# Kernel tuning notes

Hardware: AMD Instinct MI355X
Metric: run time of the kernel (lower is better)

The kernel has to match this reference:

```python
import jax, jax.numpy as jnp
import numpy as np

B, H, W = 4, 128, 128
THRESHOLD = 0.1      # hard-coded in chamfer_distance_batch
CHUNK = 2048         # row-chunk size for the online-min over the distance matrix
BIG = 1e9            # masks out inactive columns in the min-reduction
EMPTY_CHD = 1e6      # sentinel when either point set is empty (matches torch code)
EPS = 1e-12          # sqrt clamp for numerical safety


def setup_inputs() -> dict:
    key = jax.random.key(0)
    k1, k2 = jax.random.split(key)
    batch1 = jax.random.normal(k1, (B, H, W), dtype=jnp.float32)
    batch2 = jax.random.normal(k2, (B, H, W), dtype=jnp.float32)
    return {"batch1": batch1, "batch2": batch2}


def _chamfer(batch1, batch2):
    Bn, Hn, Wn = batch1.shape
    HW = Hn * Wn
    w1 = jax.nn.relu(batch1 - THRESHOLD).reshape(Bn, HW)   # [B, HW]
    w2 = jax.nn.relu(batch2 - THRESHOLD).reshape(Bn, HW)
    gy, gx = jnp.meshgrid(jnp.arange(Hn), jnp.arange(Wn), indexing='ij')
    coords = jnp.stack([gy, gx], axis=-1).reshape(HW, 2).astype(jnp.float32)  # [HW, 2]
    # torch code multiplies coords by the relu'd weights BEFORE cdist (quirk kept)
    c1 = coords[None, :, :] * w1[:, :, None]               # [B, HW, 2]
    c2 = coords[None, :, :] * w2[:, :, None]
    m1 = w1 > 0                                            # active-point masks
    m2 = w2 > 0

    def directed(cf, mf, ct, mt):
        # mean over active rows of min distance to active columns, chunked
        ct_sq = jnp.sum(ct * ct, axis=-1)                  # [HW]

        def chunk_min(cc):                                 # cc: [CHUNK, 2]
            # |a-b|^2 = |a|^2 + |b|^2 - 2 a.b  (GEMM form)
            d2 = (jnp.sum(cc * cc, axis=-1)[:, None]
                  + ct_sq[None, :]
                  - 2.0 * cc @ ct.T)                       # [CHUNK, HW]
            d = jnp.sqrt(jnp.maximum(d2, EPS))
            return jnp.min(jnp.where(mt[None, :], d, BIG), axis=1)  # [CHUNK]

        mins = jax.lax.map(chunk_min, cf.reshape(-1, CHUNK, 2)).reshape(-1)  # [HW]
        n = jnp.sum(mf)
        return jnp.sum(mins * mf) / jnp.maximum(n, 1)

    def per_image(c1b, m1b, c2b, m2b):
        chd = directed(c1b, m1b, c2b, m2b) + directed(c2b, m2b, c1b, m1b)
        nonempty = (jnp.sum(m1b) > 0) & (jnp.sum(m2b) > 0)
        return jnp.where(nonempty, chd, jnp.asarray(EMPTY_CHD, chd.dtype))

    return jax.vmap(per_image)(c1, m1, c2, m2)   # [B]


def reference(batch1, batch2):
    return _chamfer(batch1, batch2)
```

## Files before the change

kernel.cpp:

```cpp
#include <hip/hip_runtime.h>
#include <math.h>


#define B_ 4
#define HW_ 16384
#define THRESH 0.1f
#define BIGF 1e30f
#define EPS_ 1e-12f

#define SEGCAP 4096
#define NSEG 4
#define NBIN 256
#define BINSCALE 0.25f
#define BINW 4.0f
#define RG 128
#define NW 8
#define AWIN 1024
#define PD_NGRP 128

__global__ __launch_bounds__(1024)
void compact_kernel(const float* __restrict__ in1, const float* __restrict__ in2,
                    int* __restrict__ segcounts, float4* __restrict__ pts,
                    uint4* __restrict__ minarr4, int* __restrict__ histG) {
    int seg = blockIdx.x, combo = blockIdx.y;
    int b = combo >> 1, s = combo & 1;
    int tid = threadIdx.x, lane = tid & 63, wid = tid >> 6;
    const float* in = s ? in2 : in1;
    int ibase = seg * SEGCAP + tid * 4;
    float4 v = ((const float4*)(in + b * HW_))[(unsigned)ibase >> 2];
    float w0 = v.x - THRESH, w1 = v.y - THRESH, w2 = v.z - THRESH, w3 = v.w - THRESH;
    int a0 = w0 > 0.f, a1 = w1 > 0.f, a2 = w2 > 0.f, a3 = w3 > 0.f;

    unsigned int bb = __float_as_uint(BIGF);
    minarr4[(unsigned)(combo * HW_ + ibase) >> 2] = make_uint4(bb, bb, bb, bb);

    __shared__ int hist[NBIN];
    if (tid < NBIN) hist[tid] = 0;

    int c = a0 + a1 + a2 + a3;
    int incl = c;
#pragma unroll
    for (int o = 1; o < 64; o <<= 1) {
        int x = __shfl_up(incl, o, 64);
        if (lane >= o) incl += x;
    }
    int wexcl = incl - c;
    __shared__ int wtot[16], wpre[17];
    if (lane == 63) wtot[wid] = incl;
    __syncthreads();
    if (tid == 0) {
        int run = 0;
#pragma unroll
        for (int ww = 0; ww < 16; ++ww) { wpre[ww] = run; run += wtot[ww]; }
        wpre[16] = run;
    }
    __syncthreads();
    int off = wpre[wid] + wexcl;
    float4* dst = pts + combo * HW_ + seg * SEGCAP;
    float wv[4] = {w0, w1, w2, w3};
    int   av[4] = {a0, a1, a2, a3};
#pragma unroll
    for (int u = 0; u < 4; ++u) {
        if (av[u]) {
            int i = ibase + u;
            float qx = (float)(i >> 7) * wv[u];
            float qy = (float)(i & 127) * wv[u];
            float zz = qx * qx + qy * qy;
            dst[off] = make_float4(qx, qy, zz, 0.0f);
            int bin = min(NBIN - 1, (int)(sqrtf(zz) * BINSCALE));
            atomicAdd(&hist[bin], 1);
            ++off;
        }
    }
    if (tid == 0) segcounts[combo * 4 + seg] = wpre[16];
    __syncthreads();
    if (tid < NBIN)
        histG[(combo * NSEG + seg) * NBIN + tid] = hist[tid];
}

__global__ __launch_bounds__(512)
void scatter_kernel(const int* __restrict__ segcounts, const float4* __restrict__ pts,
                    const int* __restrict__ histG, float4* __restrict__ sorted,
                    int* __restrict__ binstartG) {
    int seg = blockIdx.x, combo = blockIdx.y;
    int tid = threadIdx.x;
    __shared__ int h[NSEG][NBIN];
    __shared__ int sc[NBIN];
    __shared__ int cur[NBIN];
    for (int i = tid; i < NSEG * NBIN; i += 512)
        h[i >> 8][i & 255] = histG[combo * NSEG * NBIN + i];
    __syncthreads();
    if (tid < NBIN) sc[tid] = h[0][tid] + h[1][tid] + h[2][tid] + h[3][tid];
    __syncthreads();
#pragma unroll
    for (int o = 1; o < NBIN; o <<= 1) {
        int v = (tid < NBIN && tid >= o) ? sc[tid - o] : 0;
        __syncthreads();
        if (tid < NBIN) sc[tid] += v;
        __syncthreads();
    }
    if (tid < NBIN) {
        int tot = h[0][tid] + h[1][tid] + h[2][tid] + h[3][tid];
        int excl = sc[tid] - tot;
        int o2 = excl;
        for (int s2 = 0; s2 < seg; ++s2) o2 += h[s2][tid];
        cur[tid] = o2;
        if (seg == 0) binstartG[combo * (NBIN + 1) + tid] = excl;
    }
    if (seg == 0 && tid == 0)
        binstartG[combo * (NBIN + 1) + NBIN] = sc[NBIN - 1];
    __syncthreads();
    int c = segcounts[combo * 4 + seg];
    const float4* src = pts + combo * HW_ + seg * SEGCAP;
    for (int i = tid; i < c; i += 512) {
        float4 p = src[i];
        int bin = min(NBIN - 1, (int)(sqrtf(p.z) * BINSCALE));
        int idx = atomicAdd(&cur[bin], 1);
        sorted[(size_t)combo * HW_ + idx] =
            make_float4(p.x, p.y, p.z, __uint_as_float((unsigned)(seg * SEGCAP + i)));
    }
}

__global__ __launch_bounds__(512, 4)
void pdist_kernel(const float4* __restrict__ sorted, const int* __restrict__ binstart,
                  unsigned int* __restrict__ minarr) {
    int grp = blockIdx.x, combo = blockIdx.y;
    int tid = threadIdx.x, lane = tid & 63, w = tid >> 6;
    int tc = combo ^ 1;
    int n_from = binstart[combo * (NBIN + 1) + NBIN];
    int n_to   = binstart[tc * (NBIN + 1) + NBIN];
    if (n_from <= 0 || n_to <= 0) return;
    int rbase = grp * RG;
    if (rbase >= n_from) return;

    const float4* __restrict__ rows = sorted + (size_t)combo * HW_;
    const float4* __restrict__ cols = sorted + (size_t)tc * HW_;

    int r0 = rbase + lane, r1 = rbase + 64 + lane;
    bool v0 = r0 < n_from, v1 = r1 < n_from;
    float4 P0 = rows[min(r0, n_from - 1)];
    float4 P1 = rows[min(r1, n_from - 1)];
    float npx0 = -2.0f * P0.x, npy0 = -2.0f * P0.y, p20 = P0.z;
    float npx1 = -2.0f * P1.x, npy1 = -2.0f * P1.y, p21 = P1.z;
    unsigned int slot0 = __float_as_uint(P0.w);
    unsigned int slot1 = __float_as_uint(P1.w);
    float m0 = BIGF, m1 = BIGF;

    int blo_r = min(NBIN - 1, (int)(sqrtf(rows[rbase].z) * BINSCALE));
    int bhi_r = min(NBIN - 1, (int)(sqrtf(rows[min(rbase + RG - 1, n_from - 1)].z) * BINSCALE));
    float rho_lo = (float)blo_r * BINW;
    float rho_hi = (float)(bhi_r + 1) * BINW;

    int jmid = (binstart[tc * (NBIN + 1) + blo_r]
                + binstart[tc * (NBIN + 1) + min(bhi_r + 1, NBIN)]) >> 1;
    int aHi = min(n_to, jmid + AWIN / 2);
    int aLo = max(0, aHi - AWIN);
    aHi = min(n_to, aLo + AWIN);

    __shared__ __align__(16) float bx[NW][64], by[NW][64], bz[NW][64];
    __shared__ float mW[NW][RG];

    auto ld = [&](int jb) -> float4 {
        int j = jb + lane;
        return (j < n_to) ? cols[j] : make_float4(0.0f, 0.0f, BIGF, 0.0f);
    };
    auto proc = [&](float4 qc) {
        bx[w][lane] = qc.x; by[w][lane] = qc.y; bz[w][lane] = qc.z;
        const float4* X = (const float4*)bx[w];
        const float4* Y = (const float4*)by[w];
        const float4* Z = (const float4*)bz[w];
#pragma unroll
        for (int q4 = 0; q4 < 16; ++q4) {
            float4 qx = X[q4], qy = Y[q4], qz = Z[q4];
            float t0 = fmaf(qy.x, npy0, fmaf(qx.x, npx0, qz.x));
            float u1 = fmaf(qy.y, npy0, fmaf(qx.y, npx0, qz.y));
            m0 = fminf(m0, fminf(t0, u1));
            float u2 = fmaf(qy.z, npy0, fmaf(qx.z, npx0, qz.z));
            float u3 = fmaf(qy.w, npy0, fmaf(qx.w, npx0, qz.w));
            m0 = fminf(m0, fminf(u2, u3));
            float s0 = fmaf(qy.x, npy1, fmaf(qx.x, npx1, qz.x));
            float s1 = fmaf(qy.y, npy1, fmaf(qx.y, npx1, qz.y));
            m1 = fminf(m1, fminf(s0, s1));
            float s2 = fmaf(qy.z, npy1, fmaf(qx.z, npx1, qz.z));
            float s3 = fmaf(qy.w, npy1, fmaf(qx.w, npx1, qz.w));
            m1 = fminf(m1, fminf(s2, s3));
        }
    };

    int nbA = (aHi - aLo + 63) >> 6;
    float4 qn = (w < nbA) ? ld(aLo + (w << 6))
                          : make_float4(0.0f, 0.0f, BIGF, 0.0f);
    for (int bi = w; bi < nbA; bi += NW) {
        float4 qc = qn;
        if (bi + NW < nbA) qn = ld(aLo + ((bi + NW) << 6));
        proc(qc);
    }

    mW[w][lane] = m0; mW[w][64 + lane] = m1;
    __syncthreads();
    float c0 = mW[0][lane], c1 = mW[0][64 + lane];
#pragma unroll
    for (int ww = 1; ww < NW; ++ww) {
        c0 = fminf(c0, mW[ww][lane]);
        c1 = fminf(c1, mW[ww][64 + lane]);
    }
    float md0 = v0 ? fmaxf(c0 + p20, 0.0f) : -1.0f;
    float md1 = v1 ? fmaxf(c1 + p21, 0.0f) : -1.0f;
    float g = fmaxf(md0, md1);
#pragma unroll
    for (int o = 1; o < 64; o <<= 1) g = fmaxf(g, __shfl_xor(g, o));

    float S = sqrtf((g + 1.0f) * (1.0f / 0.99f)) * 1.001f;
    int b_lo = max(0, (int)((rho_lo - S) * BINSCALE) - 1);
    int b_hi = min(NBIN, (int)((rho_hi + S) * BINSCALE) + 2);
    int jlo2 = binstart[tc * (NBIN + 1) + b_lo];
    int jhi2 = binstart[tc * (NBIN + 1) + b_hi];

    m0 = c0; m1 = c1;
    int nbL = (max(0, aLo - jlo2) + 63) >> 6;
    int nbR = (max(0, jhi2 - aHi) + 63) >> 6;
    int nbB = nbL + nbR;
    auto jbB = [&](int bi) {
        return (bi < nbL) ? (jlo2 + (bi << 6)) : (aHi + ((bi - nbL) << 6));
    };
    qn = (w < nbB) ? ld(jbB(w)) : make_float4(0.0f, 0.0f, BIGF, 0.0f);
    for (int bi = w; bi < nbB; bi += NW) {
        float4 qc = qn;
        if (bi + NW < nbB) qn = ld(jbB(bi + NW));
        proc(qc);
    }
    __syncthreads();
    mW[w][lane] = m0; mW[w][64 + lane] = m1;
    __syncthreads();
    if (w == 0) {
        float f0 = mW[0][lane], f1 = mW[0][64 + lane];
#pragma unroll
        for (int ww = 1; ww < NW; ++ww) {
            f0 = fminf(f0, mW[ww][lane]);
            f1 = fminf(f1, mW[ww][64 + lane]);
        }
        if (v0) minarr[combo * HW_ + slot0] = __float_as_uint(fmaxf(f0 + p20, 0.0f));
        if (v1) minarr[combo * HW_ + slot1] = __float_as_uint(fmaxf(f1 + p21, 0.0f));
    }
}

__global__ void reduce_out_kernel(const int* __restrict__ segcounts,
                                  const unsigned int* __restrict__ minarr,
                                  float* __restrict__ out) {
    int b = blockIdx.x;
    int tid = threadIdx.x;
    int d = tid >> 9;
    int t = tid & 511;
    int combo = b * 2 + d;

    float acc = 0.0f;
    for (int s = 0; s < NSEG; ++s) {
        int c = segcounts[combo * 4 + s];
        const unsigned int* ma = minarr + combo * HW_ + s * SEGCAP;
        for (int r = t; r < c; r += 512)
            acc += sqrtf(fmaxf(__uint_as_float(ma[r]), EPS_));
    }
#pragma unroll
    for (int o = 32; o >= 1; o >>= 1) acc += __shfl_down(acc, o);

    __shared__ float wsum[16];
    if ((tid & 63) == 0) wsum[tid >> 6] = acc;
    __syncthreads();
    if (tid == 0) {
        float s0 = 0.0f, s1 = 0.0f;
#pragma unroll
        for (int w = 0; w < 8; ++w)  s0 += wsum[w];
#pragma unroll
        for (int w = 8; w < 16; ++w) s1 += wsum[w];
        int n0 = 0, n1 = 0;
#pragma unroll
        for (int s = 0; s < NSEG; ++s) {
            n0 += segcounts[(b * 2) * 4 + s];
            n1 += segcounts[(b * 2 + 1) * 4 + s];
        }
        out[b] = (n0 > 0 && n1 > 0)
                 ? s0 / (float)n0 + s1 / (float)n1
                 : 1.0e6f;
    }
}

extern "C" void kernel_launch(void* const* d_in, const int* in_sizes, int n_in,
                              void* d_out, int out_size, void* d_ws, size_t ws_size,
                              hipStream_t stream) {
    const float* in1 = (const float*)d_in[0];
    const float* in2 = (const float*)d_in[1];
    float* out = (float*)d_out;
    char* ws = (char*)d_ws;
    int* segcounts = (int*)ws;
    float4* pts = (float4*)(ws + 256);
    size_t minoff = 256 + (size_t)8 * HW_ * sizeof(float4);
    unsigned int* minarr = (unsigned int*)(ws + minoff);
    size_t sortoff = minoff + (size_t)8 * HW_ * sizeof(unsigned int);
    float4* sorted = (float4*)(ws + sortoff);
    size_t binoff = sortoff + (size_t)8 * HW_ * sizeof(float4);
    int* binstart = (int*)(ws + binoff);
    size_t histoff = binoff + (size_t)8 * (NBIN + 1) * sizeof(int);
    int* histG = (int*)(ws + histoff);

    hipLaunchKernelGGL(compact_kernel, dim3(NSEG, 8), dim3(1024), 0, stream,
                       in1, in2, segcounts, pts, (uint4*)minarr, histG);
    hipLaunchKernelGGL(scatter_kernel, dim3(NSEG, 8), dim3(512), 0, stream,
                       segcounts, pts, histG, sorted, binstart);
    hipLaunchKernelGGL(pdist_kernel, dim3(PD_NGRP, 8), dim3(512), 0, stream,
                       sorted, binstart, minarr);
    hipLaunchKernelGGL(reduce_out_kernel, dim3(B_), dim3(1024), 0, stream,
                       segcounts, minarr, out);
}
```

Before: 83.69 us.

## Widen pdist row tiles to 8 rows per thread and split columns across z-blocks

Each thread now holds 8 row points in registers instead of 2, and each block covers 512 rows instead of 128. Every column value read from LDS is reused across more rows, which raises FMA work per LDS load. Column tiles are interleaved between two z-blocks by tile parity, and their per-row minima are merged with atomicMin into the preinitialized min array. The trade-offs are higher register pressure, an extra block-wide max reduction, fewer row groups, and a slightly different pruning bound because the tile is coarser.

```diff
diff --git a/kernel.cpp b/kernel.cpp
--- a/kernel.cpp
+++ b/kernel.cpp
@@ -13,10 +13,12 @@
 #define NBIN 256
 #define BINSCALE 0.25f
 #define BINW 4.0f
-#define RG 128
+#define RG 512
+#define RPT 8
 #define NW 8
 #define AWIN 1024
-#define PD_NGRP 128
+#define PD_NGRP 32
+#define MWS 520
 
 __global__ __launch_bounds__(1024)
 void compact_kernel(const float* __restrict__ in1, const float* __restrict__ in2,
@@ -124,7 +126,7 @@
 __global__ __launch_bounds__(512, 4)
 void pdist_kernel(const float4* __restrict__ sorted, const int* __restrict__ binstart,
                   unsigned int* __restrict__ minarr) {
-    int grp = blockIdx.x, combo = blockIdx.y;
+    int grp = blockIdx.x, combo = blockIdx.y, z = blockIdx.z;
     int tid = threadIdx.x, lane = tid & 63, w = tid >> 6;
     int tc = combo ^ 1;
     int n_from = binstart[combo * (NBIN + 1) + NBIN];
@@ -136,15 +138,13 @@
     const float4* __restrict__ rows = sorted + (size_t)combo * HW_;
     const float4* __restrict__ cols = sorted + (size_t)tc * HW_;
 
-    int r0 = rbase + lane, r1 = rbase + 64 + lane;
-    bool v0 = r0 < n_from, v1 = r1 < n_from;
-    float4 P0 = rows[min(r0, n_from - 1)];
-    float4 P1 = rows[min(r1, n_from - 1)];
-    float npx0 = -2.0f * P0.x, npy0 = -2.0f * P0.y, p20 = P0.z;
-    float npx1 = -2.0f * P1.x, npy1 = -2.0f * P1.y, p21 = P1.z;
-    unsigned int slot0 = __float_as_uint(P0.w);
-    unsigned int slot1 = __float_as_uint(P1.w);
-    float m0 = BIGF, m1 = BIGF;
+    float npx[RPT], npy[RPT], p2[RPT], m[RPT];
+#pragma unroll
+    for (int k = 0; k < RPT; ++k) {
+        int r = min(rbase + (k << 6) + lane, n_from - 1);
+        float4 P = rows[r];
+        npx[k] = -2.0f * P.x; npy[k] = -2.0f * P.y; p2[k] = P.z; m[k] = BIGF;
+    }
 
     int blo_r = min(NBIN - 1, (int)(sqrtf(rows[rbase].z) * BINSCALE));
     int bhi_r = min(NBIN - 1, (int)(sqrtf(rows[min(rbase + RG - 1, n_from - 1)].z) * BINSCALE));
@@ -153,15 +153,16 @@
 
     int jmid = (binstart[tc * (NBIN + 1) + blo_r]
                 + binstart[tc * (NBIN + 1) + min(bhi_r + 1, NBIN)]) >> 1;
-    int aHi = min(n_to, jmid + AWIN / 2);
-    int aLo = max(0, aHi - AWIN);
-    aHi = min(n_to, aLo + AWIN);
+    int tmax = (n_to + 63) >> 6;
+    int ta0 = max(0, jmid - AWIN / 2) >> 6;
+    int ta1 = min(ta0 + AWIN / 64, tmax);
 
     __shared__ __align__(16) float bx[NW][64], by[NW][64], bz[NW][64];
-    __shared__ float mW[NW][RG];
-
-    auto ld = [&](int jb) -> float4 {
-        int j = jb + lane;
+    __shared__ float mW[NW][MWS];
+    __shared__ float gW[NW];
+
+    auto ld = [&](int t) -> float4 {
+        int j = (t << 6) + lane;
         return (j < n_to) ? cols[j] : make_float4(0.0f, 0.0f, BIGF, 0.0f);
     };
     auto proc = [&](float4 qc) {
@@ -172,75 +173,73 @@
 #pragma unroll
         for (int q4 = 0; q4 < 16; ++q4) {
             float4 qx = X[q4], qy = Y[q4], qz = Z[q4];
-            float t0 = fmaf(qy.x, npy0, fmaf(qx.x, npx0, qz.x));
-            float u1 = fmaf(qy.y, npy0, fmaf(qx.y, npx0, qz.y));
-            m0 = fminf(m0, fminf(t0, u1));
-            float u2 = fmaf(qy.z, npy0, fmaf(qx.z, npx0, qz.z));
-            float u3 = fmaf(qy.w, npy0, fmaf(qx.w, npx0, qz.w));
-            m0 = fminf(m0, fminf(u2, u3));
-            float s0 = fmaf(qy.x, npy1, fmaf(qx.x, npx1, qz.x));
-            float s1 = fmaf(qy.y, npy1, fmaf(qx.y, npx1, qz.y));
-            m1 = fminf(m1, fminf(s0, s1));
-            float s2 = fmaf(qy.z, npy1, fmaf(qx.z, npx1, qz.z));
-            float s3 = fmaf(qy.w, npy1, fmaf(qx.w, npx1, qz.w));
-            m1 = fminf(m1, fminf(s2, s3));
+#pragma unroll
+            for (int k = 0; k < RPT; ++k) {
+                float t0 = fmaf(qy.x, npy[k], fmaf(qx.x, npx[k], qz.x));
+                float u1 = fmaf(qy.y, npy[k], fmaf(qx.y, npx[k], qz.y));
+                m[k] = fminf(m[k], fminf(t0, u1));
+                float u2 = fmaf(qy.z, npy[k], fmaf(qx.z, npx[k], qz.z));
+                float u3 = fmaf(qy.w, npy[k], fmaf(qx.w, npx[k], qz.w));
+                m[k] = fminf(m[k], fminf(u2, u3));
+            }
         }
     };
 
-    int nbA = (aHi - aLo + 63) >> 6;
-    float4 qn = (w < nbA) ? ld(aLo + (w << 6))
-                          : make_float4(0.0f, 0.0f, BIGF, 0.0f);
-    for (int bi = w; bi < nbA; bi += NW) {
-        float4 qc = qn;
-        if (bi + NW < nbA) qn = ld(aLo + ((bi + NW) << 6));
-        proc(qc);
-    }
-
-    mW[w][lane] = m0; mW[w][64 + lane] = m1;
-    __syncthreads();
-    float c0 = mW[0][lane], c1 = mW[0][64 + lane];
-#pragma unroll
-    for (int ww = 1; ww < NW; ++ww) {
-        c0 = fminf(c0, mW[ww][lane]);
-        c1 = fminf(c1, mW[ww][64 + lane]);
-    }
-    float md0 = v0 ? fmaxf(c0 + p20, 0.0f) : -1.0f;
-    float md1 = v1 ? fmaxf(c1 + p21, 0.0f) : -1.0f;
-    float g = fmaxf(md0, md1);
+    int tA = ta0 + ((ta0 ^ z) & 1);
+    for (int t = tA + 2 * w; t < ta1; t += 2 * NW) proc(ld(t));
+
+#pragma unroll
+    for (int k = 0; k < RPT; ++k) mW[w][(k << 6) + lane] = m[k];
+    __syncthreads();
+    int myrow = (w << 6) + lane;
+    float cmin = mW[0][myrow];
+#pragma unroll
+    for (int ww = 1; ww < NW; ++ww) cmin = fminf(cmin, mW[ww][myrow]);
+    float md = (rbase + myrow < n_from) ? fmaxf(cmin + p2[w], 0.0f) : -1.0f;
+    float g = md;
 #pragma unroll
     for (int o = 1; o < 64; o <<= 1) g = fmaxf(g, __shfl_xor(g, o));
+    if (lane == 0) gW[w] = g;
+    __syncthreads();
+    g = gW[0];
+#pragma unroll
+    for (int ww = 1; ww < NW; ++ww) g = fmaxf(g, gW[ww]);
 
     float S = sqrtf((g + 1.0f) * (1.0f / 0.99f)) * 1.001f;
     int b_lo = max(0, (int)((rho_lo - S) * BINSCALE) - 1);
     int b_hi = min(NBIN, (int)((rho_hi + S) * BINSCALE) + 2);
     int jlo2 = binstart[tc * (NBIN + 1) + b_lo];
     int jhi2 = binstart[tc * (NBIN + 1) + b_hi];
-
-    m0 = c0; m1 = c1;
-    int nbL = (max(0, aLo - jlo2) + 63) >> 6;
-    int nbR = (max(0, jhi2 - aHi) + 63) >> 6;
-    int nbB = nbL + nbR;
-    auto jbB = [&](int bi) {
-        return (bi < nbL) ? (jlo2 + (bi << 6)) : (aHi + ((bi - nbL) << 6));
+    int tb_lo = jlo2 >> 6;
+    int tb_hi = min((jhi2 + 63) >> 6, tmax);
+
+    int tL0 = tb_lo + ((tb_lo ^ z) & 1);
+    int nL = max(0, (ta0 - tL0 + 1) >> 1);
+    int tR0 = ta1 + ((ta1 ^ z) & 1);
+    int nR = max(0, (tb_hi - tR0 + 1) >> 1);
+    int nB = nL + nR;
+    auto jbB = [&](int u) {
+        return (u < nL) ? (tL0 + 2 * u) : (tR0 + 2 * (u - nL));
     };
-    qn = (w < nbB) ? ld(jbB(w)) : make_float4(0.0f, 0.0f, BIGF, 0.0f);
-    for (int bi = w; bi < nbB; bi += NW) {
+
+    float4 qn = (w < nB) ? ld(jbB(w)) : make_float4(0.0f, 0.0f, BIGF, 0.0f);
+    for (int u = w; u < nB; u += NW) {
         float4 qc = qn;
-        if (bi + NW < nbB) qn = ld(jbB(bi + NW));
+        if (u + NW < nB) qn = ld(jbB(u + NW));
         proc(qc);
     }
-    __syncthreads();
-    mW[w][lane] = m0; mW[w][64 + lane] = m1;
-    __syncthreads();
-    if (w == 0) {
-        float f0 = mW[0][lane], f1 = mW[0][64 + lane];
-#pragma unroll
-        for (int ww = 1; ww < NW; ++ww) {
-            f0 = fminf(f0, mW[ww][lane]);
-            f1 = fminf(f1, mW[ww][64 + lane]);
-        }
-        if (v0) minarr[combo * HW_ + slot0] = __float_as_uint(fmaxf(f0 + p20, 0.0f));
-        if (v1) minarr[combo * HW_ + slot1] = __float_as_uint(fmaxf(f1 + p21, 0.0f));
+
+#pragma unroll
+    for (int k = 0; k < RPT; ++k) mW[w][(k << 6) + lane] = m[k];
+    __syncthreads();
+    float fm = mW[0][myrow];
+#pragma unroll
+    for (int ww = 1; ww < NW; ++ww) fm = fminf(fm, mW[ww][myrow]);
+    int grow = rbase + myrow;
+    if (grow < n_from) {
+        unsigned int slot = __float_as_uint(rows[grow].w);
+        float d2 = fmaxf(fm + p2[w], 0.0f);
+        atomicMin(&minarr[combo * HW_ + slot], __float_as_uint(d2));
     }
 }
 
@@ -306,7 +305,7 @@
                        in1, in2, segcounts, pts, (uint4*)minarr, histG);
     hipLaunchKernelGGL(scatter_kernel, dim3(NSEG, 8), dim3(512), 0, stream,
                        segcounts, pts, histG, sorted, binstart);
-    hipLaunchKernelGGL(pdist_kernel, dim3(PD_NGRP, 8), dim3(512), 0, stream,
+    hipLaunchKernelGGL(pdist_kernel, dim3(PD_NGRP, 8, 2), dim3(512), 0, stream,
                        sorted, binstart, minarr);
     hipLaunchKernelGGL(reduce_out_kernel, dim3(B_), dim3(1024), 0, stream,
                        segcounts, minarr, out);
```

Result: slower. 103.8 us (+24.0%).
